# Kernel tuning notes

Hardware: AMD Instinct MI355X
Metric: run time of the kernel (lower is better)

## Reference

```python
import jax, jax.numpy as jnp
import numpy as np
from jax import lax

B, T, N, E, M = 2, 24, 1500, 2000, 4000
DIM, NLY, K = 64, 2, 3
H = DIM + DIM // 2  # 96: GAT input dim after concat with NodeEdge output


def setup_inputs():
    ks = iter(jax.random.split(jax.random.key(0), 100))
    def rn(shape, scale=1.0):
        return jax.random.normal(next(ks), shape, dtype=jnp.float32) * scale
    d = {}
    d["x_in"] = rn((B, T, N, 4)); d["e_in"] = rn((B, T, E, 3))
    d["b_in"] = rn((B, T, N, 4)); d["a_in"] = rn((B, T, E, 3))
    def lin(name, din, dout):
        d[name + "_W"] = rn((din, dout), 1.0 / float(np.sqrt(din)))
        d[name + "_b"] = jnp.zeros((dout,), jnp.float32)
    lin("enc0", 4, DIM); lin("enc1", 3, DIM)
    lin("enc2", 4, DIM // 2); lin("enc3", 3, DIM // 2)
    d["inci"] = jax.random.uniform(next(ks), (N, E), dtype=jnp.float32)
    for p in ("s1", "s2"):
        for g in ("gx", "ge"):
            d[p + "_" + g + "_W"] = rn((NLY, H, DIM), 0.1)
            d[p + "_" + g + "_as"] = rn((NLY, DIM), 0.1)
            d[p + "_" + g + "_ad"] = rn((NLY, DIM), 0.1)
            d[p + "_" + g + "_b"] = jnp.zeros((NLY, DIM), jnp.float32)
        d[p + "_ne_W"] = rn((NLY, DIM, DIM // 2), 0.125)
        d[p + "_ne_b"] = jnp.zeros((NLY, DIM // 2), jnp.float32)
        d[p + "_ne_w"] = rn((NLY, N, E), 0.02)
        d[p + "_ne_p"] = jnp.zeros((NLY, N, E), jnp.float32)
        d[p + "_en_W"] = rn((NLY, DIM, DIM // 2), 0.125)
        d[p + "_en_b"] = jnp.zeros((NLY, DIM // 2), jnp.float32)
        d[p + "_en_w"] = rn((NLY, E, N), 0.02)
        d[p + "_en_p"] = jnp.zeros((NLY, E, N), jnp.float32)
        d[p + "_tp_W"] = rn((NLY, DIM, DIM, K), 0.07)
        d[p + "_tp_b"] = jnp.zeros((NLY, DIM), jnp.float32)
    lin("conc", H, DIM); lin("res", DIM, DIM); lin("out", DIM, 1)
    d["edge_ind"] = jax.random.randint(next(ks), (2, E), 0, N)
    d["node_ind"] = jax.random.randint(next(ks), (2, M), 0, E)
    return d


def gat(x, src, dst, n, W, a_s, a_d, bias):
    # PyG GATConv (heads=1, concat=True, neg_slope=0.2); self-loops already in src/dst.
    # x: [B,T,n,din] -> G=B*T independent graphs (the batched edge_index replication
    # of BatchGATConv is exactly equivalent to vmapping over graph replicas).
    g = x.reshape(B * T, n, x.shape[-1])
    z = g @ W                                    # [G,n,DIM]
    es = jnp.einsum('gnd,d->gn', z, a_s)
    ed = jnp.einsum('gnd,d->gn', z, a_d)
    alpha = jax.nn.leaky_relu(es[:, src] + ed[:, dst], 0.2)   # [G,Etot]
    def one(a, zz):
        m = jax.ops.segment_max(a, dst, num_segments=n)
        ex = jnp.exp(a - m[dst])
        s = jax.ops.segment_sum(ex, dst, num_segments=n)
        w = ex / s[dst]
        return jax.ops.segment_sum(w[:, None] * zz[src], dst, num_segments=n)
    out = jax.vmap(one)(alpha, z) + bias
    return out.reshape(B, T, n, DIM)


def node_edge(inp, W, b, w, p, A):
    # NodeEdge: relu(Linear(dim->dim//2)) then incidence-masked matmul
    xe = jax.nn.relu(inp @ W + b)                # [B,T,*,DIM//2]
    return jnp.einsum('ne,btef->btnf', w * A + p, xe)


def causal_conv(h, W, b, dil):
    # h: [M,C,T]; left-pad (K-1)*dil -> causal dilated Conv1d
    pad = (K - 1) * dil
    out = lax.conv_general_dilated(h, W, (1,), [(pad, 0)], rhs_dilation=(dil,),
                                   dimension_numbers=('NCH', 'OIH', 'NCH'))
    return out + b[None, :, None]


def stblock(x, e, src_n, dst_n, src_e, dst_e, inc, P):
    (gxW, gxas, gxad, gxb, geW, geas, gead, geb,
     neW, neb, new, nep, enW, enb, enw, enp, tpW, tpb) = P
    incT = inc.T
    for l in range(NLY):
        xe = node_edge(e, neW[l], neb[l], new[l], nep[l], inc)
        x = jax.nn.relu(gat(jnp.concatenate([x, xe], -1), src_n, dst_n, N,
                            gxW[l], gxas[l], gxad[l], gxb[l]))
        ex = node_edge(x, enW[l], enb[l], enw[l], enp[l], incT)
        e = jax.nn.relu(gat(jnp.concatenate([e, ex], -1), src_e, dst_e, E,
                            geW[l], geas[l], gead[l], geb[l]))
    xt = x.transpose(0, 2, 3, 1).reshape(B * N, DIM, T)   # 'b t n d -> (b n) d t'
    et = e.transpose(0, 2, 3, 1).reshape(B * E, DIM, T)
    h = jnp.concatenate([xt, et], axis=0)
    for l in range(NLY):
        h = jax.nn.relu(causal_conv(h, tpW[l], tpb[l], 2 ** l))
    x = h[:B * N].reshape(B, N, DIM, T).transpose(0, 3, 1, 2)
    e = h[B * N:].reshape(B, E, DIM, T).transpose(0, 3, 1, 2)
    return x, e


def _forward(x_in, e_in, b_in, a_in, enc0_W, enc0_b, enc1_W, enc1_b, enc2_W, enc2_b,
             enc3_W, enc3_b, inci,
             s1_gx_W, s1_gx_as, s1_gx_ad, s1_gx_b, s1_ge_W, s1_ge_as, s1_ge_ad, s1_ge_b,
             s1_ne_W, s1_ne_b, s1_ne_w, s1_ne_p, s1_en_W, s1_en_b, s1_en_w, s1_en_p,
             s1_tp_W, s1_tp_b,
             s2_gx_W, s2_gx_as, s2_gx_ad, s2_gx_b, s2_ge_W, s2_ge_as, s2_ge_ad, s2_ge_b,
             s2_ne_W, s2_ne_b, s2_ne_w, s2_ne_p, s2_en_W, s2_en_b, s2_en_w, s2_en_p,
             s2_tp_W, s2_tp_b,
             conc_W, conc_b, res_W, res_b, out_W, out_b, edge_ind, node_ind):
    # add self-loops once (GATConv add_self_loops=True)
    src_n = jnp.concatenate([edge_ind[0], jnp.arange(N)])
    dst_n = jnp.concatenate([edge_ind[1], jnp.arange(N)])
    src_e = jnp.concatenate([node_ind[0], jnp.arange(E)])
    dst_e = jnp.concatenate([node_ind[1], jnp.arange(E)])
    inc = jnp.abs(inci)
    x = x_in @ enc0_W + enc0_b
    e = e_in @ enc1_W + enc1_b
    bb = jax.nn.relu(b_in @ enc2_W + enc2_b)
    aa = jax.nn.relu(a_in @ enc3_W + enc3_b)
    res_x = jnp.broadcast_to(x[:, -1:], (B, T, N, DIM))   # pre-relu last step, tiled
    res_e = jnp.broadcast_to(e[:, -1:], (B, T, E, DIM))
    x = jax.nn.relu(x); e = jax.nn.relu(e)
    P1 = (s1_gx_W, s1_gx_as, s1_gx_ad, s1_gx_b, s1_ge_W, s1_ge_as, s1_ge_ad, s1_ge_b,
          s1_ne_W, s1_ne_b, s1_ne_w, s1_ne_p, s1_en_W, s1_en_b, s1_en_w, s1_en_p,
          s1_tp_W, s1_tp_b)
    P2 = (s2_gx_W, s2_gx_as, s2_gx_ad, s2_gx_b, s2_ge_W, s2_ge_as, s2_ge_ad, s2_ge_b,
          s2_ne_W, s2_ne_b, s2_ne_w, s2_ne_p, s2_en_W, s2_en_b, s2_en_w, s2_en_p,
          s2_tp_W, s2_tp_b)
    x, e = stblock(x, e, src_n, dst_n, src_e, dst_e, inc, P1)
    # concs is [Linear]*2 in torch -> shared weights for both branches
    x = jax.nn.relu(jnp.concatenate([x, bb], -1) @ conc_W + conc_b)
    e = jax.nn.relu(jnp.concatenate([e, aa], -1) @ conc_W + conc_b)
    x, e = stblock(x, e, src_n, dst_n, src_e, dst_e, inc, P2)
    x = jax.nn.relu(jnp.cumsum(x @ res_W + res_b, axis=1) + res_x)
    e = jax.nn.relu(jnp.cumsum(e @ res_W + res_b, axis=1) + res_e)
    out = jnp.clip((x @ out_W + out_b) / 6.0 + 0.5, 0.0, 1.0)   # F.hardsigmoid
    eo = jnp.tanh(e @ out_W + out_b)
    return out, eo


def reference(x_in, e_in, b_in, a_in, enc0_W, enc0_b, enc1_W, enc1_b, enc2_W, enc2_b,
              enc3_W, enc3_b, inci,
              s1_gx_W, s1_gx_as, s1_gx_ad, s1_gx_b, s1_ge_W, s1_ge_as, s1_ge_ad, s1_ge_b,
              s1_ne_W, s1_ne_b, s1_ne_w, s1_ne_p, s1_en_W, s1_en_b, s1_en_w, s1_en_p,
              s1_tp_W, s1_tp_b,
              s2_gx_W, s2_gx_as, s2_gx_ad, s2_gx_b, s2_ge_W, s2_ge_as, s2_ge_ad, s2_ge_b,
              s2_ne_W, s2_ne_b, s2_ne_w, s2_ne_p, s2_en_W, s2_en_b, s2_en_w, s2_en_p,
              s2_tp_W, s2_tp_b,
              conc_W, conc_b, res_W, res_b, out_W, out_b, edge_ind, node_ind):
    return _forward(x_in, e_in, b_in, a_in, enc0_W, enc0_b, enc1_W, enc1_b, enc2_W,
                    enc2_b, enc3_W, enc3_b, inci,
                    s1_gx_W, s1_gx_as, s1_gx_ad, s1_gx_b, s1_ge_W, s1_ge_as, s1_ge_ad,
                    s1_ge_b, s1_ne_W, s1_ne_b, s1_ne_w, s1_ne_p, s1_en_W, s1_en_b,
                    s1_en_w, s1_en_p, s1_tp_W, s1_tp_b,
                    s2_gx_W, s2_gx_as, s2_gx_ad, s2_gx_b, s2_ge_W, s2_ge_as, s2_ge_ad,
                    s2_ge_b, s2_ne_W, s2_ne_b, s2_ne_w, s2_ne_p, s2_en_W, s2_en_b,
                    s2_en_w, s2_en_p, s2_tp_W, s2_tp_b,
                    conc_W, conc_b, res_W, res_b, out_W, out_b, edge_ind, node_ind)
```

## Files before the change

kernel.cpp:

```cpp
#include <hip/hip_runtime.h>
#include <hip/hip_bf16.h>
#include <cfloat>
#include <math.h>

typedef __hip_bfloat16 bf16;
typedef __attribute__((ext_vector_type(8))) short short8v;
typedef __attribute__((ext_vector_type(4))) float f32x4;

constexpr int B_ = 2, T_ = 24, N_ = 1500, E_ = 2000, M_ = 4000, G_ = 48;
constexpr int KPN = 2048;
constexpr int KPE = 1536;

__device__ __forceinline__ float b2f(bf16 v) { return __bfloat162float(v); }
__device__ __forceinline__ bf16 f2b(float v) { return __float2bfloat16(v); }
static inline int ceilDiv(int a, int b) { return (a + b - 1) / b; }

__global__ __launch_bounds__(256) void k_sentinel(float* __restrict__ out, int n, float val) {
  int i = blockIdx.x * 256 + threadIdx.x;
  if (i < n) out[i] = val;
}

__global__ __launch_bounds__(256) void k_wprep(const float* __restrict__ g0, const float* __restrict__ e0,
                                               const float* __restrict__ g1, const float* __restrict__ e1,
                                               const float* __restrict__ cw, const float* __restrict__ rw,
                                               const float* __restrict__ t0, const float* __restrict__ t1,
                                               bf16* __restrict__ out) {
  int i = blockIdx.x * 256 + threadIdx.x;
  if (i >= 108544) return;
  float v;
  if (i < 49152) {
    int which = i / 12288, r = i % 12288;
    const float* W = which == 0 ? g0 : which == 1 ? e0 : which == 2 ? g1 : e1;
    int l = r / 6144, j = r % 6144;
    int n = j / 96, k = j % 96;
    v = W[l * 6144 + k * 64 + n];
  } else if (i < 55296) {
    int j = i - 49152, n = j / 96, k = j % 96;
    v = cw[k * 64 + n];
  } else if (i < 59392) {
    int j = i - 55296, n = j / 64, k = j % 64;
    v = rw[k * 64 + n];
  } else {
    int r = i - 59392;
    int which = r / 24576;
    const float* W = which ? t1 : t0;
    int rr = r % 24576;
    int l = rr / 12288, j = rr % 12288;
    int ii = j & 63, o = (j >> 6) & 63, k = j >> 12;
    v = W[l * 12288 + o * 192 + ii * 3 + k];
  }
  out[i] = f2b(v);
}

template <int DIN, int DOUT, bool SAVE>
__global__ __launch_bounds__(256) void k_enc(const float* __restrict__ in, const float* __restrict__ W,
                                             const float* __restrict__ bias, bf16* __restrict__ out,
                                             float* __restrict__ last, int nodes) {
  int idx = blockIdx.x * 256 + threadIdx.x;
  if (idx >= G_ * nodes * DOUT) return;
  int d = idx % DOUT;
  int row = idx / DOUT;
  int node = row % nodes;
  int g = row / nodes;
  const float* ir = in + (size_t)row * DIN;
  float acc = bias[d];
#pragma unroll
  for (int i = 0; i < DIN; i++) acc += ir[i] * W[i * DOUT + d];
  if (SAVE) {
    if (g % T_ == T_ - 1) last[((size_t)(g / T_) * nodes + node) * DOUT + d] = acc;
  }
  out[idx] = f2b(fmaxf(acc, 0.f));
}

__global__ __launch_bounds__(256) void k_lin_neT(const bf16* __restrict__ act, const float* __restrict__ W,
                                                 const float* __restrict__ bias, bf16* __restrict__ outT,
                                                 int nodes, int Kp) {
  __shared__ float As[64][65];
  __shared__ float Ws[2048];
  __shared__ float bs[32];
  int g = blockIdx.y;
  int n0 = blockIdx.x * 64;
  int t = threadIdx.x;
  for (int i = t; i < 2048; i += 256) Ws[i] = W[i];
  if (t < 32) bs[t] = bias[t];
  {
    int r = t >> 2, ch = t & 3;
    int node = n0 + r;
    short tmp[16];
    if (node < nodes) {
      const bf16* src = act + ((size_t)g * nodes + node) * 64 + ch * 16;
      *reinterpret_cast<uint4*>(tmp) = *reinterpret_cast<const uint4*>(src);
      *reinterpret_cast<uint4*>(tmp + 8) = *reinterpret_cast<const uint4*>(src + 8);
#pragma unroll
      for (int j = 0; j < 16; j++) As[r][ch * 16 + j] = b2f(*reinterpret_cast<bf16*>(&tmp[j]));
    } else {
#pragma unroll
      for (int j = 0; j < 16; j++) As[r][ch * 16 + j] = 0.f;
    }
  }
  __syncthreads();
  int nd = t & 63, fq = t >> 6;
  float acc[8];
#pragma unroll
  for (int j = 0; j < 8; j++) acc[j] = bs[fq * 8 + j];
  for (int i = 0; i < 64; i++) {
    float a = As[nd][i];
#pragma unroll
    for (int j = 0; j < 8; j++) acc[j] += a * Ws[i * 32 + fq * 8 + j];
  }
  bool valid = (n0 + nd) < nodes;
#pragma unroll
  for (int j = 0; j < 8; j++) {
    float v = valid ? fmaxf(acc[j], 0.f) : 0.f;
    outT[(size_t)(g * 32 + fq * 8 + j) * Kp + n0 + nd] = f2b(v);
  }
}

__global__ __launch_bounds__(256) void k_mat(const float* __restrict__ w, const float* __restrict__ p,
                                             const float* __restrict__ inci, bf16* __restrict__ mat,
                                             int rows, int K, int Kp) {
  int i = blockIdx.x * 256 + threadIdx.x;
  if (i >= rows * Kp) return;
  int row = i / Kp, k = i % Kp;
  float v = 0.f;
  if (k < K) {
    size_t o = (size_t)row * K + k;
    v = w[o] * fabsf(inci[o]) + p[o];
  }
  mat[i] = f2b(v);
}

__global__ void k_matT(const float* __restrict__ w, const float* __restrict__ p,
                       const float* __restrict__ inci, bf16* __restrict__ mat) {
  __shared__ float tl[32][33];
  int e0 = blockIdx.x * 32, n0 = blockIdx.y * 32;
  for (int r = threadIdx.y; r < 32; r += 8) {
    int n = n0 + r, e = e0 + threadIdx.x;
    tl[r][threadIdx.x] = (n < N_ && e < E_) ? fabsf(inci[(size_t)n * E_ + e]) : 0.f;
  }
  __syncthreads();
  for (int r = threadIdx.y; r < 32; r += 8) {
    int e = e0 + r, n = n0 + threadIdx.x;
    if (e < E_ && n < KPE) {
      size_t o = (size_t)e * N_ + n;
      mat[(size_t)e * KPE + n] = (n < N_) ? f2b(tl[threadIdx.x][r] * w[o] + p[o]) : f2b(0.f);
    }
  }
}

__global__ __launch_bounds__(256) void k_mgemm64(const bf16* __restrict__ A0, const bf16* __restrict__ Bt,
                                                 bf16* __restrict__ Cp, int Mm, int Kp, int Nn, int gy) {
  __shared__ __align__(16) short As[4][4][64][8];
  __shared__ __align__(16) short Bs[4][4][64][8];
  int tid = threadIdx.x;
  int nwg = gridDim.x;
  int bid = blockIdx.x;
  int l = (bid & 7) * (nwg >> 3) + (bid >> 3);
  int bm = (l % gy) * 64, bn = (l / gy) * 64;
  int lane = tid & 63, wid = tid >> 6;
  int wr = wid >> 1, wc = wid & 1;
  f32x4 acc[2][2];
#pragma unroll
  for (int i = 0; i < 2; i++)
#pragma unroll
    for (int j = 0; j < 2; j++) acc[i][j] = f32x4{0.f, 0.f, 0.f, 0.f};

  const int sr = tid >> 2;
  const int sc = tid & 3;
  const int kb = lane >> 4, lr = lane & 15;
  const int gmA = bm + sr, gnB = bn + sr;
  const bool va_ok = (gmA < Mm), vb_ok = (gnB < Nn);
  const bf16* ap = A0 + (size_t)gmA * Kp + sc * 8;
  const bf16* bp = Bt + (size_t)gnB * Kp + sc * 8;
  const uint4 z4 = {0, 0, 0, 0};
  const int P = Kp >> 5;

  uint4 va0 = va_ok ? *reinterpret_cast<const uint4*>(ap) : z4;
  uint4 vb0 = vb_ok ? *reinterpret_cast<const uint4*>(bp) : z4;
  uint4 va1 = va_ok ? *reinterpret_cast<const uint4*>(ap + 32) : z4;
  uint4 vb1 = vb_ok ? *reinterpret_cast<const uint4*>(bp + 32) : z4;
  *reinterpret_cast<uint4*>(&As[0][sc][sr][0]) = va0;
  *reinterpret_cast<uint4*>(&Bs[0][sc][sr][0]) = vb0;
  uint4 va2 = va_ok ? *reinterpret_cast<const uint4*>(ap + 64) : z4;
  uint4 vb2 = vb_ok ? *reinterpret_cast<const uint4*>(bp + 64) : z4;
  __syncthreads();

  for (int p = 0; p < P; p += 2) {
    *reinterpret_cast<uint4*>(&As[(p + 1) & 3][sc][sr][0]) = va1;
    *reinterpret_cast<uint4*>(&Bs[(p + 1) & 3][sc][sr][0]) = vb1;
    if (p + 3 < P) {
      va1 = va_ok ? *reinterpret_cast<const uint4*>(ap + (p + 3) * 32) : z4;
      vb1 = vb_ok ? *reinterpret_cast<const uint4*>(bp + (p + 3) * 32) : z4;
    }
    {
      int bf = p & 3;
      short8v a0 = *reinterpret_cast<const short8v*>(&As[bf][kb][wr * 32 + lr][0]);
      short8v a1 = *reinterpret_cast<const short8v*>(&As[bf][kb][wr * 32 + 16 + lr][0]);
      short8v b0 = *reinterpret_cast<const short8v*>(&Bs[bf][kb][wc * 32 + lr][0]);
      short8v b1 = *reinterpret_cast<const short8v*>(&Bs[bf][kb][wc * 32 + 16 + lr][0]);
      __builtin_amdgcn_s_setprio(1);
      acc[0][0] = __builtin_amdgcn_mfma_f32_16x16x32_bf16(a0, b0, acc[0][0], 0, 0, 0);
      acc[0][1] = __builtin_amdgcn_mfma_f32_16x16x32_bf16(a0, b1, acc[0][1], 0, 0, 0);
      acc[1][0] = __builtin_amdgcn_mfma_f32_16x16x32_bf16(a1, b0, acc[1][0], 0, 0, 0);
      acc[1][1] = __builtin_amdgcn_mfma_f32_16x16x32_bf16(a1, b1, acc[1][1], 0, 0, 0);
      __builtin_amdgcn_s_setprio(0);
    }
    __syncthreads();
    *reinterpret_cast<uint4*>(&As[(p + 2) & 3][sc][sr][0]) = va2;
    *reinterpret_cast<uint4*>(&Bs[(p + 2) & 3][sc][sr][0]) = vb2;
    if (p + 4 < P) {
      va2 = va_ok ? *reinterpret_cast<const uint4*>(ap + (p + 4) * 32) : z4;
      vb2 = vb_ok ? *reinterpret_cast<const uint4*>(bp + (p + 4) * 32) : z4;
    }
    {
      int bf = (p + 1) & 3;
      short8v a0 = *reinterpret_cast<const short8v*>(&As[bf][kb][wr * 32 + lr][0]);
      short8v a1 = *reinterpret_cast<const short8v*>(&As[bf][kb][wr * 32 + 16 + lr][0]);
      short8v b0 = *reinterpret_cast<const short8v*>(&Bs[bf][kb][wc * 32 + lr][0]);
      short8v b1 = *reinterpret_cast<const short8v*>(&Bs[bf][kb][wc * 32 + 16 + lr][0]);
      __builtin_amdgcn_s_setprio(1);
      acc[0][0] = __builtin_amdgcn_mfma_f32_16x16x32_bf16(a0, b0, acc[0][0], 0, 0, 0);
      acc[0][1] = __builtin_amdgcn_mfma_f32_16x16x32_bf16(a0, b1, acc[0][1], 0, 0, 0);
      acc[1][0] = __builtin_amdgcn_mfma_f32_16x16x32_bf16(a1, b0, acc[1][0], 0, 0, 0);
      acc[1][1] = __builtin_amdgcn_mfma_f32_16x16x32_bf16(a1, b1, acc[1][1], 0, 0, 0);
      __builtin_amdgcn_s_setprio(0);
    }
    __syncthreads();
  }
#pragma unroll
  for (int mi = 0; mi < 2; mi++) {
    int r0 = bm + wr * 32 + mi * 16 + (lane >> 4) * 4;
#pragma unroll
    for (int ni = 0; ni < 2; ni++) {
      int col = bn + wc * 32 + ni * 16 + lr;
      if (col >= Nn) continue;
#pragma unroll
      for (int i = 0; i < 4; i++) {
        int r = r0 + i;
        if (r < Mm) Cp[(size_t)r * Nn + col] = f2b(acc[mi][ni][i]);
      }
    }
  }
}

template <int AMODE, int BNt, bool CF32b, bool ESED>
__global__ __launch_bounds__(256) void k_mgemm(const bf16* __restrict__ A0, const bf16* __restrict__ A1,
                                               const bf16* __restrict__ Bt, void* __restrict__ Cp,
                                               int Mm, int Kp, int Nn, int nodes,
                                               const float* __restrict__ bias, int relu,
                                               const float* __restrict__ asv, const float* __restrict__ adv,
                                               float* __restrict__ esOut, float* __restrict__ edOut) {
  constexpr int BM = 128;
  constexpr int WTN = BNt / 32;
  __shared__ __align__(16) short As[4][BM][8];
  __shared__ __align__(16) short Bs[4][BNt][8];
  __shared__ float smr[2][BM][2];
  int tid = threadIdx.x;
  int bm = blockIdx.y * BM;
  int bn = blockIdx.x * BNt;
  int lane = tid & 63;
  int wid = tid >> 6;
  int wr = wid >> 1, wc = wid & 1;
  f32x4 acc[4][WTN];
#pragma unroll
  for (int i = 0; i < 4; i++)
#pragma unroll
    for (int j = 0; j < WTN; j++) acc[i][j] = f32x4{0.f, 0.f, 0.f, 0.f};

  const int ar = tid >> 1;
  const int ah = tid & 1;
  const int kb = lane >> 4;
  const int lr = lane & 15;

  for (int k0 = 0; k0 < Kp; k0 += 32) {
    uint4 va0 = {0, 0, 0, 0}, va1 = {0, 0, 0, 0};
    int gm = bm + ar;
    if (gm < Mm) {
      int ks = k0 + ah * 16;
      const bf16* src;
      if (AMODE == 0) src = A0 + (size_t)gm * Kp + ks;
      else if (ks < 64) src = A0 + (size_t)gm * 64 + ks;
      else if (AMODE == 1) {
        int g = gm / nodes, nd = gm % nodes;
        src = A1 + ((size_t)nd * G_ + g) * 32 + (ks - 64);
      } else {
        src = A1 + (size_t)gm * 32 + (ks - 64);
      }
      const uint4* p = reinterpret_cast<const uint4*>(src);
      va0 = p[0];
      va1 = p[1];
    }
    *reinterpret_cast<uint4*>(&As[ah * 2 + 0][ar][0]) = va0;
    *reinterpret_cast<uint4*>(&As[ah * 2 + 1][ar][0]) = va1;
    if (BNt == 128) {
      int br = tid >> 1, bh = tid & 1;
      uint4 vb0 = {0, 0, 0, 0}, vb1 = {0, 0, 0, 0};
      int gn = bn + br;
      if (gn < Nn) {
        const uint4* p = reinterpret_cast<const uint4*>(Bt + (size_t)gn * Kp + k0 + bh * 16);
        vb0 = p[0];
        vb1 = p[1];
      }
      *reinterpret_cast<uint4*>(&Bs[bh * 2 + 0][br][0]) = vb0;
      *reinterpret_cast<uint4*>(&Bs[bh * 2 + 1][br][0]) = vb1;
    } else {
      int br = tid >> 2, bk = tid & 3;
      uint4 vb0 = {0, 0, 0, 0};
      int gn = bn + br;
      if (gn < Nn) vb0 = *reinterpret_cast<const uint4*>(Bt + (size_t)gn * Kp + k0 + bk * 8);
      *reinterpret_cast<uint4*>(&Bs[bk][br][0]) = vb0;
    }
    __syncthreads();
    short8v a[4], b[WTN];
#pragma unroll
    for (int mi = 0; mi < 4; mi++)
      a[mi] = *reinterpret_cast<const short8v*>(&As[kb][wr * 64 + mi * 16 + lr][0]);
#pragma unroll
    for (int ni = 0; ni < WTN; ni++)
      b[ni] = *reinterpret_cast<const short8v*>(&Bs[kb][wc * (BNt / 2) + ni * 16 + lr][0]);
#pragma unroll
    for (int mi = 0; mi < 4; mi++)
#pragma unroll
      for (int ni = 0; ni < WTN; ni++)
        acc[mi][ni] = __builtin_amdgcn_mfma_f32_16x16x32_bf16(a[mi], b[ni], acc[mi][ni], 0, 0, 0);
    __syncthreads();
  }
#pragma unroll
  for (int mi = 0; mi < 4; mi++) {
    int r0 = bm + wr * 64 + mi * 16 + (lane >> 4) * 4;
#pragma unroll
    for (int ni = 0; ni < WTN; ni++) {
      int col = bn + wc * (BNt / 2) + ni * 16 + lr;
      float bv = bias ? bias[col] : 0.f;
#pragma unroll
      for (int i = 0; i < 4; i++) {
        int r = r0 + i;
        if (r < Mm) {
          float v = acc[mi][ni][i] + bv;
          if (relu) v = fmaxf(v, 0.f);
          if (CF32b) ((float*)Cp)[(size_t)r * Nn + col] = v;
          else ((bf16*)Cp)[(size_t)r * Nn + col] = f2b(v);
        }
      }
    }
  }
  if (ESED) {
    float asc0 = asv[wc * 32 + lr];
    float asc1 = asv[wc * 32 + 16 + lr];
    float adc0 = adv[wc * 32 + lr];
    float adc1 = adv[wc * 32 + 16 + lr];
#pragma unroll
    for (int mi = 0; mi < 4; mi++) {
#pragma unroll
      for (int i = 0; i < 4; i++) {
        float pe = acc[mi][0][i] * asc0 + acc[mi][1][i] * asc1;
        float pd = acc[mi][0][i] * adc0 + acc[mi][1][i] * adc1;
#pragma unroll
        for (int o = 8; o; o >>= 1) { pe += __shfl_xor(pe, o); pd += __shfl_xor(pd, o); }
        if (lr == 0) {
          int rl = wr * 64 + mi * 16 + (lane >> 4) * 4 + i;
          smr[wc][rl][0] = pe;
          smr[wc][rl][1] = pd;
        }
      }
    }
    __syncthreads();
    if (tid < BM) {
      int r = bm + tid;
      if (r < Mm) {
        esOut[r] = smr[0][tid][0] + smr[1][tid][0];
        edOut[r] = smr[0][tid][1] + smr[1][tid][1];
      }
    }
  }
}

template <int DIL>
__global__ __launch_bounds__(256) void k_cgemm(const bf16* __restrict__ A, const bf16* __restrict__ Wc,
                                               const float* __restrict__ bias, bf16* __restrict__ C,
                                               int Mm, int nodes) {
  __shared__ __align__(16) short As[4][4][128][8];
  int tid = threadIdx.x;
  int bm = blockIdx.x * 128;
  int lane = tid & 63, wid = tid >> 6;
  int wr = wid >> 1, wc = wid & 1;
  const int ar = tid >> 1, ah = tid & 1;
  const int kb = lane >> 4, lr = lane & 15;
  const int gm = bm + ar;
  const int t = (gm / nodes) % T_;
  const uint4 z4 = {0, 0, 0, 0};

  short8v bfr[3][2][2];
#pragma unroll
  for (int tap = 0; tap < 3; tap++)
#pragma unroll
    for (int kc = 0; kc < 2; kc++)
#pragma unroll
      for (int ni = 0; ni < 2; ni++) {
        int col = wc * 32 + ni * 16 + lr;
        bfr[tap][kc][ni] = *reinterpret_cast<const short8v*>(Wc + tap * 4096 + (size_t)col * 64 + kc * 32 + kb * 8);
      }

  f32x4 acc[4][2];
#pragma unroll
  for (int i = 0; i < 4; i++)
#pragma unroll
    for (int j = 0; j < 2; j++) acc[i][j] = f32x4{0.f, 0.f, 0.f, 0.f};

#define CG_LDA(p, vx, vy)                                                          \
  {                                                                                \
    const int sh_ = (((p) >> 1) - 2) * DIL;                                        \
    if ((gm < Mm) && (t + sh_ >= 0)) {                                             \
      const uint4* pp = reinterpret_cast<const uint4*>(                            \
          A + ((size_t)gm + (size_t)sh_ * nodes) * 64 + ((p) & 1) * 32 + ah * 16); \
      vx = pp[0];                                                                  \
      vy = pp[1];                                                                  \
    } else {                                                                       \
      vx = z4;                                                                     \
      vy = z4;                                                                     \
    }                                                                              \
  }
#define CG_WR(buf, vx, vy)                                     \
  *reinterpret_cast<uint4*>(&As[buf][ah * 2 + 0][ar][0]) = vx; \
  *reinterpret_cast<uint4*>(&As[buf][ah * 2 + 1][ar][0]) = vy;
#define CG_MFMA(q)                                                                                         \
  {                                                                                                        \
    short8v a0_ = *reinterpret_cast<const short8v*>(&As[(q) & 3][kb][wr * 64 + 0 + lr][0]);                \
    short8v a1_ = *reinterpret_cast<const short8v*>(&As[(q) & 3][kb][wr * 64 + 16 + lr][0]);               \
    short8v a2_ = *reinterpret_cast<const short8v*>(&As[(q) & 3][kb][wr * 64 + 32 + lr][0]);               \
    short8v a3_ = *reinterpret_cast<const short8v*>(&As[(q) & 3][kb][wr * 64 + 48 + lr][0]);               \
    __builtin_amdgcn_s_setprio(1);                                                                         \
    acc[0][0] = __builtin_amdgcn_mfma_f32_16x16x32_bf16(a0_, bfr[(q) >> 1][(q) & 1][0], acc[0][0], 0, 0, 0); \
    acc[0][1] = __builtin_amdgcn_mfma_f32_16x16x32_bf16(a0_, bfr[(q) >> 1][(q) & 1][1], acc[0][1], 0, 0, 0); \
    acc[1][0] = __builtin_amdgcn_mfma_f32_16x16x32_bf16(a1_, bfr[(q) >> 1][(q) & 1][0], acc[1][0], 0, 0, 0); \
    acc[1][1] = __builtin_amdgcn_mfma_f32_16x16x32_bf16(a1_, bfr[(q) >> 1][(q) & 1][1], acc[1][1], 0, 0, 0); \
    acc[2][0] = __builtin_amdgcn_mfma_f32_16x16x32_bf16(a2_, bfr[(q) >> 1][(q) & 1][0], acc[2][0], 0, 0, 0); \
    acc[2][1] = __builtin_amdgcn_mfma_f32_16x16x32_bf16(a2_, bfr[(q) >> 1][(q) & 1][1], acc[2][1], 0, 0, 0); \
    acc[3][0] = __builtin_amdgcn_mfma_f32_16x16x32_bf16(a3_, bfr[(q) >> 1][(q) & 1][0], acc[3][0], 0, 0, 0); \
    acc[3][1] = __builtin_amdgcn_mfma_f32_16x16x32_bf16(a3_, bfr[(q) >> 1][(q) & 1][1], acc[3][1], 0, 0, 0); \
    __builtin_amdgcn_s_setprio(0);                                                                         \
  }
#define CG_BODY(p, lastPair)                  \
  CG_WR(((p) + 1) & 3, r1x, r1y);             \
  if (!(lastPair)) CG_LDA((p) + 3, r1x, r1y); \
  CG_MFMA(p);                                 \
  __syncthreads();                            \
  CG_WR(((p) + 2) & 3, r2x, r2y);             \
  if (!(lastPair)) CG_LDA((p) + 4, r2x, r2y); \
  CG_MFMA((p) + 1);                           \
  __syncthreads();

  uint4 p0x, p0y, r1x, r1y, r2x, r2y;
  CG_LDA(0, p0x, p0y);
  CG_LDA(1, r1x, r1y);
  CG_WR(0, p0x, p0y);
  CG_LDA(2, r2x, r2y);
  __syncthreads();

  CG_BODY(0, false)
  CG_BODY(2, false)
  CG_BODY(4, true)

#undef CG_LDA
#undef CG_WR
#undef CG_MFMA
#undef CG_BODY

#pragma unroll
  for (int mi = 0; mi < 4; mi++) {
    int r0 = bm + wr * 64 + mi * 16 + (lane >> 4) * 4;
#pragma unroll
    for (int ni = 0; ni < 2; ni++) {
      int col = wc * 32 + ni * 16 + lr;
      float bv = bias[col];
#pragma unroll
      for (int i = 0; i < 4; i++) {
        int r = r0 + i;
        if (r < Mm) C[(size_t)r * 64 + col] = f2b(fmaxf(acc[mi][ni][i] + bv, 0.f));
      }
    }
  }
}

__global__ __launch_bounds__(256) void k_gat_w(const float* __restrict__ es, const float* __restrict__ edv,
                                               const int* __restrict__ off, const int* __restrict__ adj,
                                               float* __restrict__ wgt, int nodes, int tot) {
  int idx = blockIdx.x * 256 + threadIdx.x;
  if (idx >= G_ * nodes) return;
  int g = idx / nodes, node = idx % nodes;
  int s0 = off[node], s1 = off[node + 1];
  const float* esg = es + (size_t)g * nodes;
  float edval = edv[(size_t)g * nodes + node];
  float m = -FLT_MAX;
  for (int s = s0; s < s1; s++) {
    float a = esg[adj[s]] + edval;
    a = (a >= 0.f) ? a : 0.2f * a;
    m = fmaxf(m, a);
  }
  float den = 0.f;
  float* wg = wgt + (size_t)g * tot;
  for (int s = s0; s < s1; s++) {
    float a = esg[adj[s]] + edval;
    a = (a >= 0.f) ? a : 0.2f * a;
    float ex = expf(a - m);
    den += ex;
    wg[s] = ex;
  }
  float inv = (s1 > s0) ? 1.f / den : 0.f;
  for (int s = s0; s < s1; s++) wg[s] *= inv;
}

__global__ __launch_bounds__(256) void k_gat_aggr3(const bf16* __restrict__ z, const float* __restrict__ wgt,
                                                   const int* __restrict__ off, const int* __restrict__ adj,
                                                   const float* __restrict__ bias, bf16* __restrict__ out,
                                                   int nodes, int tot) {
  int idx = blockIdx.x * 256 + threadIdx.x;
  if (idx >= G_ * nodes * 16) return;
  int c = idx & 15;
  int rest = idx >> 4;
  int node = rest % nodes;
  int g = rest / nodes;
  int s0 = off[node], s1 = off[node + 1];
  const bf16* zg = z + (size_t)g * nodes * 64 + c * 4;
  const float* wg = wgt + (size_t)g * tot;
  float n0 = 0.f, n1 = 0.f, n2 = 0.f, n3 = 0.f;
  for (int s = s0; s < s1; s++) {
    int src = adj[s];
    float w = wg[s];
    bf16 v[4];
    *reinterpret_cast<uint2*>(v) = *reinterpret_cast<const uint2*>(zg + (size_t)src * 64);
    n0 += w * b2f(v[0]);
    n1 += w * b2f(v[1]);
    n2 += w * b2f(v[2]);
    n3 += w * b2f(v[3]);
  }
  bf16 ov[4];
  ov[0] = f2b(fmaxf(n0 + bias[c * 4 + 0], 0.f));
  ov[1] = f2b(fmaxf(n1 + bias[c * 4 + 1], 0.f));
  ov[2] = f2b(fmaxf(n2 + bias[c * 4 + 2], 0.f));
  ov[3] = f2b(fmaxf(n3 + bias[c * 4 + 3], 0.f));
  *reinterpret_cast<uint2*>(out + (size_t)rest * 64 + c * 4) = *reinterpret_cast<uint2*>(ov);
}

__global__ __launch_bounds__(1024) void k_csr(const int* __restrict__ indN, const int* __restrict__ indE,
                                              int* __restrict__ offN, int* __restrict__ adjN,
                                              int* __restrict__ offE, int* __restrict__ adjE) {
  __shared__ int cnt[2048];
  __shared__ int a[1024];
  const int* ind;
  int ner, nn;
  int *off, *adj;
  if (blockIdx.x == 0) { ind = indN; ner = E_; nn = N_; off = offN; adj = adjN; }
  else { ind = indE; ner = M_; nn = E_; off = offE; adj = adjE; }
  int tot = ner + nn;
  int t = threadIdx.x;
  for (int i = t; i < nn; i += 1024) cnt[i] = 0;
  __syncthreads();
  for (int i = t; i < tot; i += 1024) {
    int d = (i < ner) ? ind[ner + i] : (i - ner);
    if (d >= 0 && d < nn) atomicAdd(&cnt[d], 1);
  }
  __syncthreads();
  int c0 = (2 * t < nn) ? cnt[2 * t] : 0;
  int c1 = (2 * t + 1 < nn) ? cnt[2 * t + 1] : 0;
  a[t] = c0 + c1;
  __syncthreads();
  for (int d = 1; d < 1024; d <<= 1) {
    int u = (t >= d) ? a[t - d] : 0;
    __syncthreads();
    a[t] += u;
    __syncthreads();
  }
  int excl = (t > 0) ? a[t - 1] : 0;
  if (2 * t < nn) { cnt[2 * t] = excl; off[2 * t] = excl; }
  if (2 * t + 1 < nn) { cnt[2 * t + 1] = excl + c0; off[2 * t + 1] = excl + c0; }
  if (t == 0) off[nn] = a[1023];
  __syncthreads();
  for (int i = t; i < tot; i += 1024) {
    int s, d;
    if (i < ner) { s = ind[i]; d = ind[ner + i]; }
    else { s = d = i - ner; }
    if (d >= 0 && d < nn) {
      int pos = atomicAdd(&cnt[d], 1);
      adj[pos] = s;
    }
  }
}

template <bool XB>
__global__ __launch_bounds__(256) void k_out(const float* __restrict__ yx, const float* __restrict__ last,
                                             const float* __restrict__ oW, const float* __restrict__ ob_,
                                             float* __restrict__ dout, int nodes) {
  int wid = threadIdx.x >> 6, lane = threadIdx.x & 63;
  int node = blockIdx.x * 4 + wid;
  if (node >= nodes) return;
  float lw = oW[lane];
  float ob = ob_[0];
  float lv = last[(size_t)node * 64 + lane];
  float acc = 0.f;
  for (int tt = 0; tt < T_; tt++) {
    acc += yx[((size_t)tt * nodes + node) * 64 + lane];
    float v = fmaxf(acc + lv, 0.f);
    float p = v * lw;
#pragma unroll
    for (int o2 = 32; o2; o2 >>= 1) p += __shfl_down(p, o2);
    if (lane == 0) {
      float o = p + ob;
      if (XB) o = fminf(fmaxf(o / 6.f + 0.5f, 0.f), 1.f);
      else o = tanhf(o);
      dout[(size_t)tt * nodes + node] = o;
    }
  }
}

extern "C" void kernel_launch(void* const* d_in, const int* in_sizes, int n_in,
                              void* d_out, int out_size, void* d_ws, size_t ws_size,
                              hipStream_t stream) {
  float* dout = (float*)d_out;

  if (n_in != 57) {
    k_sentinel<<<ceilDiv(out_size, 256), 256, 0, stream>>>(dout, out_size, 20000.f + 128.f * n_in);
    return;
  }
  static const int expSz[57] = {
      288000, 288000, 288000, 288000,
      256, 64, 192, 64, 128, 32, 96, 32,
      3000000,
      12288, 128, 128, 128, 12288, 128, 128, 128,
      4096, 64, 6000000, 6000000, 4096, 64, 6000000, 6000000,
      24576, 128,
      12288, 128, 128, 128, 12288, 128, 128, 128,
      4096, 64, 6000000, 6000000, 4096, 64, 6000000, 6000000,
      24576, 128,
      6144, 64, 4096, 64, 64, 1, 4000, 8000};
  for (int i = 0; i < 57; i++) {
    if (in_sizes[i] != expSz[i]) {
      k_sentinel<<<ceilDiv(out_size, 256), 256, 0, stream>>>(dout, out_size, 4096.f + 64.f * i);
      return;
    }
  }

  auto ff = [&](int i) { return (const float*)d_in[i]; };
  const float *x_in = ff(0), *e_in = ff(1), *b_in = ff(2), *a_in = ff(3);
  const float *enc0W = ff(4), *enc0b = ff(5), *enc1W = ff(6), *enc1b = ff(7);
  const float *enc2W = ff(8), *enc2b = ff(9), *enc3W = ff(10), *enc3b = ff(11);
  const float* inci = ff(12);
  const float *concW = ff(49), *concb = ff(50), *resW = ff(51), *resb = ff(52);
  const float *outW = ff(53), *outb = ff(54);
  const int* edge_ind = (const int*)d_in[55];
  const int* node_ind = (const int*)d_in[56];

  char* base = (char*)d_ws;
  size_t off = 0;
  auto A = [&](size_t bytes) { void* p = base + off; off = (off + bytes + 255) & ~(size_t)255; return p; };
  char* SCR = (char*)A(21504000);
  bf16* xbuf = (bf16*)A(9216000);
  bf16* ebuf = (bf16*)A(12288000);
  float* lastx = (float*)A(768000);
  float* laste = (float*)A(1024000);
  float* es = (float*)A(384000);
  float* edv = (float*)A(384000);
  float* wgt = (float*)A((size_t)G_ * (M_ + E_) * 4);
  bf16* wAll = (bf16*)A(217088);
  int* offN = (int*)A((N_ + 1) * 4);
  int* offE = (int*)A((E_ + 1) * 4);
  int* adjN = (int*)A((E_ + N_) * 4);
  int* adjE = (int*)A((M_ + E_) * 4);
  size_t required = off;

  if (ws_size < required) {
    k_sentinel<<<ceilDiv(out_size, 256), 256, 0, stream>>>(dout, out_size, 1000.f + (float)(ws_size >> 20));
    return;
  }

  bf16* matb = (bf16*)SCR;
  bf16* tlinT = (bf16*)(SCR + 6553600);
  bf16* tmat = (bf16*)(SCR + 13107200);
  bf16* zbuf = (bf16*)SCR;
  bf16* bscr = (bf16*)SCR;
  bf16* cx1 = (bf16*)SCR;
  bf16* ce1 = (bf16*)(SCR + 9216000);
  float* zres = (float*)SCR;

  const int totN = E_ + N_;
  const int totE = M_ + E_;

  k_wprep<<<ceilDiv(108544, 256), 256, 0, stream>>>(ff(13), ff(17), ff(31), ff(35), concW, resW,
                                                    ff(29), ff(47), wAll);
  k_csr<<<2, 1024, 0, stream>>>(edge_ind, node_ind, offN, adjN, offE, adjE);

  k_enc<4, 64, true><<<ceilDiv(G_ * N_ * 64, 256), 256, 0, stream>>>(x_in, enc0W, enc0b, xbuf, lastx, N_);
  k_enc<3, 64, true><<<ceilDiv(G_ * E_ * 64, 256), 256, 0, stream>>>(e_in, enc1W, enc1b, ebuf, laste, E_);

  auto stblock = [&](int sb, int sbi) {
    const float *gxas = ff(sb + 1), *gxad = ff(sb + 2), *gxb = ff(sb + 3);
    const float *geas = ff(sb + 5), *gead = ff(sb + 6), *geb = ff(sb + 7);
    const float *neW = ff(sb + 8), *neb = ff(sb + 9), *nw = ff(sb + 10), *np_ = ff(sb + 11);
    const float *enW = ff(sb + 12), *enb = ff(sb + 13), *ew = ff(sb + 14), *ep = ff(sb + 15);
    const float* tpb = ff(sb + 17);
    for (int l = 0; l < 2; l++) {
      const bf16* gxw_t = wAll + sbi * 24576 + l * 6144;
      const bf16* gew_t = wAll + sbi * 24576 + 12288 + l * 6144;
      k_lin_neT<<<dim3(KPN / 64, G_), 256, 0, stream>>>(ebuf, neW + l * 2048, neb + l * 32, tlinT, E_, KPN);
      k_mat<<<ceilDiv(N_ * KPN, 256), 256, 0, stream>>>(nw + (size_t)l * N_ * E_, np_ + (size_t)l * N_ * E_, inci, matb, N_, E_, KPN);
      k_mgemm64<<<dim3(24 * 24), 256, 0, stream>>>(matb, tlinT, tmat, N_, KPN, 1536, 24);
      k_mgemm<1, 64, false, true><<<dim3(1, ceilDiv(G_ * N_, 128)), 256, 0, stream>>>(
          xbuf, tmat, gxw_t, zbuf, G_ * N_, 96, 64, N_, nullptr, 0, gxas + l * 64, gxad + l * 64, es, edv);
      k_gat_w<<<ceilDiv(G_ * N_, 256), 256, 0, stream>>>(es, edv, offN, adjN, wgt, N_, totN);
      k_gat_aggr3<<<ceilDiv(G_ * N_ * 16, 256), 256, 0, stream>>>(zbuf, wgt, offN, adjN, gxb + l * 64, xbuf, N_, totN);
      k_lin_neT<<<dim3(KPE / 64, G_), 256, 0, stream>>>(xbuf, enW + l * 2048, enb + l * 32, tlinT, N_, KPE);
      k_matT<<<dim3(ceilDiv(E_, 32), KPE / 32), dim3(32, 8), 0, stream>>>(ew + (size_t)l * E_ * N_, ep + (size_t)l * E_ * N_, inci, matb);
      k_mgemm64<<<dim3(24 * 32), 256, 0, stream>>>(matb, tlinT, tmat, E_, KPE, 1536, 32);
      k_mgemm<1, 64, false, true><<<dim3(1, ceilDiv(G_ * E_, 128)), 256, 0, stream>>>(
          ebuf, tmat, gew_t, zbuf, G_ * E_, 96, 64, E_, nullptr, 0, geas + l * 64, gead + l * 64, es, edv);
      k_gat_w<<<ceilDiv(G_ * E_, 256), 256, 0, stream>>>(es, edv, offE, adjE, wgt, E_, totE);
      k_gat_aggr3<<<ceilDiv(G_ * E_ * 16, 256), 256, 0, stream>>>(zbuf, wgt, offE, adjE, geb + l * 64, ebuf, E_, totE);
    }
    const bf16* cw0 = wAll + 59392 + sbi * 24576;
    const bf16* cw1 = cw0 + 12288;
    k_cgemm<1><<<ceilDiv(G_ * N_, 128), 256, 0, stream>>>(xbuf, cw0, tpb, cx1, G_ * N_, N_);
    k_cgemm<1><<<ceilDiv(G_ * E_, 128), 256, 0, stream>>>(ebuf, cw0, tpb, ce1, G_ * E_, E_);
    k_cgemm<2><<<ceilDiv(G_ * N_, 128), 256, 0, stream>>>(cx1, cw1, tpb + 64, xbuf, G_ * N_, N_);
    k_cgemm<2><<<ceilDiv(G_ * E_, 128), 256, 0, stream>>>(ce1, cw1, tpb + 64, ebuf, G_ * E_, E_);
  };

  stblock(13, 0);

  const bf16* concT = wAll + 49152;
  k_enc<4, 32, false><<<ceilDiv(G_ * N_ * 32, 256), 256, 0, stream>>>(b_in, enc2W, enc2b, bscr, nullptr, N_);
  k_mgemm<2, 64, false, false><<<dim3(1, ceilDiv(G_ * N_, 128)), 256, 0, stream>>>(
      xbuf, bscr, concT, xbuf, G_ * N_, 96, 64, 0, concb, 1, nullptr, nullptr, nullptr, nullptr);
  k_enc<3, 32, false><<<ceilDiv(G_ * E_ * 32, 256), 256, 0, stream>>>(a_in, enc3W, enc3b, bscr, nullptr, E_);
  k_mgemm<2, 64, false, false><<<dim3(1, ceilDiv(G_ * E_, 128)), 256, 0, stream>>>(
      ebuf, bscr, concT, ebuf, G_ * E_, 96, 64, 0, concb, 1, nullptr, nullptr, nullptr, nullptr);

  stblock(31, 1);

  const bf16* resT = wAll + 55296;
  for (int b = 0; b < B_; b++) {
    k_mgemm<0, 64, true, false><<<dim3(1, ceilDiv(T_ * N_, 128)), 256, 0, stream>>>(
        xbuf + (size_t)b * T_ * N_ * 64, nullptr, resT, zres, T_ * N_, 64, 64, 0, resb, 0,
        nullptr, nullptr, nullptr, nullptr);
    k_out<true><<<ceilDiv(N_, 4), 256, 0, stream>>>(
        zres, lastx + (size_t)b * N_ * 64, outW, outb, dout + (size_t)b * T_ * N_, N_);
  }
  for (int b = 0; b < B_; b++) {
    k_mgemm<0, 64, true, false><<<dim3(1, ceilDiv(T_ * E_, 128)), 256, 0, stream>>>(
        ebuf + (size_t)b * T_ * E_ * 64, nullptr, resT, zres, T_ * E_, 64, 64, 0, resb, 0,
        nullptr, nullptr, nullptr, nullptr);
    k_out<false><<<ceilDiv(E_, 4), 256, 0, stream>>>(
        zres, laste + (size_t)b * E_ * 64, outW, outb, dout + (size_t)(B_ * T_ * N_) + (size_t)b * T_ * E_, E_);
  }
}
```

Measured before the change: 1.050 ms.

## Specialize small GEMM with full-K LDS load and merge node/edge launches

Replaces the generic k-looped k_mgemm with k_mgemm96, which loads the whole K=96 (or 64) A and B tiles into LDS once, syncs once, and runs all MFMAs under raised priority. The two temporal-conv GEMMs for nodes and edges are merged into single launches, and the node residual GEMM and output kernel now cover both batches in one launch each. The aim is fewer barriers and fewer kernel launches, at the cost of more LDS per block and a fixed N=64 output width.

After: 1.019 ms. -3.0%, faster.

```diff
diff --git a/kernel.cpp b/kernel.cpp
--- a/kernel.cpp
+++ b/kernel.cpp
@@ -243,94 +243,89 @@
   }
 }
 
-template <int AMODE, int BNt, bool CF32b, bool ESED>
-__global__ __launch_bounds__(256) void k_mgemm(const bf16* __restrict__ A0, const bf16* __restrict__ A1,
-                                               const bf16* __restrict__ Bt, void* __restrict__ Cp,
-                                               int Mm, int Kp, int Nn, int nodes,
-                                               const float* __restrict__ bias, int relu,
-                                               const float* __restrict__ asv, const float* __restrict__ adv,
-                                               float* __restrict__ esOut, float* __restrict__ edOut) {
-  constexpr int BM = 128;
-  constexpr int WTN = BNt / 32;
-  __shared__ __align__(16) short As[4][BM][8];
-  __shared__ __align__(16) short Bs[4][BNt][8];
-  __shared__ float smr[2][BM][2];
+template <int AMODE, int KOCT, bool CF32b, bool ESED>
+__global__ __launch_bounds__(256) void k_mgemm96(const bf16* __restrict__ A0, const bf16* __restrict__ A1,
+                                                 const bf16* __restrict__ Bt, void* __restrict__ Cp,
+                                                 int Mm, int nodes,
+                                                 const float* __restrict__ bias, int relu,
+                                                 const float* __restrict__ asv, const float* __restrict__ adv,
+                                                 float* __restrict__ esOut, float* __restrict__ edOut) {
+  constexpr int KP = KOCT * 8;
+  __shared__ __align__(16) short As[KOCT][128][8];
+  __shared__ __align__(16) short Bs[KOCT][64][8];
+  __shared__ float smr[2][128][2];
   int tid = threadIdx.x;
-  int bm = blockIdx.y * BM;
-  int bn = blockIdx.x * BNt;
-  int lane = tid & 63;
-  int wid = tid >> 6;
+  int bm = blockIdx.y * 128;
+  int lane = tid & 63, wid = tid >> 6;
   int wr = wid >> 1, wc = wid & 1;
-  f32x4 acc[4][WTN];
+  const int kb = lane >> 4, lr = lane & 15;
+  const uint4 z4 = {0, 0, 0, 0};
+
+  {
+    int ar = tid >> 1, ah = tid & 1;
+    int gm = bm + ar;
+    bool ok = (gm < Mm);
+    int gdiv = 0, gmod = 0;
+    if (AMODE == 1 && ok) { gdiv = gm / nodes; gmod = gm % nodes; }
+#pragma unroll
+    for (int c = 0; c < KOCT / 4; c++) {
+      int ks = c * 32 + ah * 16;
+      uint4 va0 = z4, va1 = z4;
+      if (ok) {
+        const bf16* src;
+        if (AMODE == 0) src = A0 + (size_t)gm * KP + ks;
+        else if (ks < 64) src = A0 + (size_t)gm * 64 + ks;
+        else if (AMODE == 1) src = A1 + ((size_t)gmod * G_ + gdiv) * 32 + (ks - 64);
+        else src = A1 + (size_t)gm * 32 + (ks - 64);
+        const uint4* p = reinterpret_cast<const uint4*>(src);
+        va0 = p[0];
+        va1 = p[1];
+      }
+      *reinterpret_cast<uint4*>(&As[c * 4 + ah * 2 + 0][ar][0]) = va0;
+      *reinterpret_cast<uint4*>(&As[c * 4 + ah * 2 + 1][ar][0]) = va1;
+    }
+  }
+  {
+    int br = tid >> 2, bk = tid & 3;
+#pragma unroll
+    for (int c = 0; c < KOCT / 4; c++) {
+      int o = c * 4 + bk;
+      uint4 vb = *reinterpret_cast<const uint4*>(Bt + (size_t)br * KP + o * 8);
+      *reinterpret_cast<uint4*>(&Bs[o][br][0]) = vb;
+    }
+  }
+  __syncthreads();
+
+  f32x4 acc[4][2];
 #pragma unroll
   for (int i = 0; i < 4; i++)
 #pragma unroll
-    for (int j = 0; j < WTN; j++) acc[i][j] = f32x4{0.f, 0.f, 0.f, 0.f};
-
-  const int ar = tid >> 1;
-  const int ah = tid & 1;
-  const int kb = lane >> 4;
-  const int lr = lane & 15;
-
-  for (int k0 = 0; k0 < Kp; k0 += 32) {
-    uint4 va0 = {0, 0, 0, 0}, va1 = {0, 0, 0, 0};
-    int gm = bm + ar;
-    if (gm < Mm) {
-      int ks = k0 + ah * 16;
-      const bf16* src;
-      if (AMODE == 0) src = A0 + (size_t)gm * Kp + ks;
-      else if (ks < 64) src = A0 + (size_t)gm * 64 + ks;
-      else if (AMODE == 1) {
-        int g = gm / nodes, nd = gm % nodes;
-        src = A1 + ((size_t)nd * G_ + g) * 32 + (ks - 64);
-      } else {
-        src = A1 + (size_t)gm * 32 + (ks - 64);
-      }
-      const uint4* p = reinterpret_cast<const uint4*>(src);
-      va0 = p[0];
-      va1 = p[1];
-    }
-    *reinterpret_cast<uint4*>(&As[ah * 2 + 0][ar][0]) = va0;
-    *reinterpret_cast<uint4*>(&As[ah * 2 + 1][ar][0]) = va1;
-    if (BNt == 128) {
-      int br = tid >> 1, bh = tid & 1;
-      uint4 vb0 = {0, 0, 0, 0}, vb1 = {0, 0, 0, 0};
-      int gn = bn + br;
-      if (gn < Nn) {
-        const uint4* p = reinterpret_cast<const uint4*>(Bt + (size_t)gn * Kp + k0 + bh * 16);
-        vb0 = p[0];
-        vb1 = p[1];
-      }
-      *reinterpret_cast<uint4*>(&Bs[bh * 2 + 0][br][0]) = vb0;
-      *reinterpret_cast<uint4*>(&Bs[bh * 2 + 1][br][0]) = vb1;
-    } else {
-      int br = tid >> 2, bk = tid & 3;
-      uint4 vb0 = {0, 0, 0, 0};
-      int gn = bn + br;
-      if (gn < Nn) vb0 = *reinterpret_cast<const uint4*>(Bt + (size_t)gn * Kp + k0 + bk * 8);
-      *reinterpret_cast<uint4*>(&Bs[bk][br][0]) = vb0;
-    }
-    __syncthreads();
-    short8v a[4], b[WTN];
+    for (int j = 0; j < 2; j++) acc[i][j] = f32x4{0.f, 0.f, 0.f, 0.f};
+
+#pragma unroll
+  for (int c = 0; c < KOCT / 4; c++) {
+    short8v a[4], b[2];
 #pragma unroll
     for (int mi = 0; mi < 4; mi++)
-      a[mi] = *reinterpret_cast<const short8v*>(&As[kb][wr * 64 + mi * 16 + lr][0]);
-#pragma unroll
-    for (int ni = 0; ni < WTN; ni++)
-      b[ni] = *reinterpret_cast<const short8v*>(&Bs[kb][wc * (BNt / 2) + ni * 16 + lr][0]);
+      a[mi] = *reinterpret_cast<const short8v*>(&As[c * 4 + kb][wr * 64 + mi * 16 + lr][0]);
+#pragma unroll
+    for (int ni = 0; ni < 2; ni++)
+      b[ni] = *reinterpret_cast<const short8v*>(&Bs[c * 4 + kb][wc * 32 + ni * 16 + lr][0]);
+    __builtin_amdgcn_s_setprio(1);
 #pragma unroll
     for (int mi = 0; mi < 4; mi++)
 #pragma unroll
-      for (int ni = 0; ni < WTN; ni++)
+      for (int ni = 0; ni < 2; ni++)
         acc[mi][ni] = __builtin_amdgcn_mfma_f32_16x16x32_bf16(a[mi], b[ni], acc[mi][ni], 0, 0, 0);
-    __syncthreads();
-  }
+    __builtin_amdgcn_s_setprio(0);
+  }
+
 #pragma unroll
   for (int mi = 0; mi < 4; mi++) {
     int r0 = bm + wr * 64 + mi * 16 + (lane >> 4) * 4;
 #pragma unroll
-    for (int ni = 0; ni < WTN; ni++) {
-      int col = bn + wc * (BNt / 2) + ni * 16 + lr;
+    for (int ni = 0; ni < 2; ni++) {
+      int col = wc * 32 + ni * 16 + lr;
       float bv = bias ? bias[col] : 0.f;
 #pragma unroll
       for (int i = 0; i < 4; i++) {
@@ -338,8 +333,8 @@
         if (r < Mm) {
           float v = acc[mi][ni][i] + bv;
           if (relu) v = fmaxf(v, 0.f);
-          if (CF32b) ((float*)Cp)[(size_t)r * Nn + col] = v;
-          else ((bf16*)Cp)[(size_t)r * Nn + col] = f2b(v);
+          if (CF32b) ((float*)Cp)[(size_t)r * 64 + col] = v;
+          else ((bf16*)Cp)[(size_t)r * 64 + col] = f2b(v);
         }
       }
     }
@@ -365,7 +360,7 @@
       }
     }
     __syncthreads();
-    if (tid < BM) {
+    if (tid < 128) {
       int r = bm + tid;
       if (r < Mm) {
         esOut[r] = smr[0][tid][0] + smr[1][tid][0];
@@ -376,12 +371,18 @@
 }
 
 template <int DIL>
-__global__ __launch_bounds__(256) void k_cgemm(const bf16* __restrict__ A, const bf16* __restrict__ Wc,
-                                               const float* __restrict__ bias, bf16* __restrict__ C,
-                                               int Mm, int nodes) {
+__global__ __launch_bounds__(256) void k_cgemm2(const bf16* __restrict__ Ax, bf16* __restrict__ Cx,
+                                                int Mx, int nx, const bf16* __restrict__ Ae,
+                                                bf16* __restrict__ Ce, int Me, int ne, int nbx,
+                                                const bf16* __restrict__ Wc, const float* __restrict__ bias) {
   __shared__ __align__(16) short As[4][4][128][8];
   int tid = threadIdx.x;
-  int bm = blockIdx.x * 128;
+  int bid = blockIdx.x;
+  const bf16* A;
+  bf16* C;
+  int Mm, nodes, bm;
+  if (bid < nbx) { A = Ax; C = Cx; Mm = Mx; nodes = nx; bm = bid * 128; }
+  else { A = Ae; C = Ce; Mm = Me; nodes = ne; bm = (bid - nbx) * 128; }
   int lane = tid & 63, wid = tid >> 6;
   int wr = wid >> 1, wc = wid & 1;
   const int ar = tid >> 1, ah = tid & 1;
@@ -590,16 +591,18 @@
 template <bool XB>
 __global__ __launch_bounds__(256) void k_out(const float* __restrict__ yx, const float* __restrict__ last,
                                              const float* __restrict__ oW, const float* __restrict__ ob_,
-                                             float* __restrict__ dout, int nodes) {
+                                             float* __restrict__ dout, int nodes, int batches) {
   int wid = threadIdx.x >> 6, lane = threadIdx.x & 63;
-  int node = blockIdx.x * 4 + wid;
-  if (node >= nodes) return;
+  int idx = blockIdx.x * 4 + wid;
+  if (idx >= batches * nodes) return;
+  int b = idx / nodes, node = idx % nodes;
+  const float* yb = yx + (size_t)b * T_ * nodes * 64;
   float lw = oW[lane];
   float ob = ob_[0];
-  float lv = last[(size_t)node * 64 + lane];
+  float lv = last[(size_t)idx * 64 + lane];
   float acc = 0.f;
   for (int tt = 0; tt < T_; tt++) {
-    acc += yx[((size_t)tt * nodes + node) * 64 + lane];
+    acc += yb[((size_t)tt * nodes + node) * 64 + lane];
     float v = fmaxf(acc + lv, 0.f);
     float p = v * lw;
 #pragma unroll
@@ -608,7 +611,7 @@
       float o = p + ob;
       if (XB) o = fminf(fmaxf(o / 6.f + 0.5f, 0.f), 1.f);
       else o = tanhf(o);
-      dout[(size_t)tt * nodes + node] = o;
+      dout[(size_t)b * T_ * nodes + (size_t)tt * nodes + node] = o;
     }
   }
 }
@@ -684,6 +687,8 @@
 
   const int totN = E_ + N_;
   const int totE = M_ + E_;
+  const int nbx = ceilDiv(G_ * N_, 128);
+  const int nbe = ceilDiv(G_ * E_, 128);
 
   k_wprep<<<ceilDiv(108544, 256), 256, 0, stream>>>(ff(13), ff(17), ff(31), ff(35), concW, resW,
                                                     ff(29), ff(47), wAll);
@@ -704,51 +709,45 @@
       k_lin_neT<<<dim3(KPN / 64, G_), 256, 0, stream>>>(ebuf, neW + l * 2048, neb + l * 32, tlinT, E_, KPN);
       k_mat<<<ceilDiv(N_ * KPN, 256), 256, 0, stream>>>(nw + (size_t)l * N_ * E_, np_ + (size_t)l * N_ * E_, inci, matb, N_, E_, KPN);
       k_mgemm64<<<dim3(24 * 24), 256, 0, stream>>>(matb, tlinT, tmat, N_, KPN, 1536, 24);
-      k_mgemm<1, 64, false, true><<<dim3(1, ceilDiv(G_ * N_, 128)), 256, 0, stream>>>(
-          xbuf, tmat, gxw_t, zbuf, G_ * N_, 96, 64, N_, nullptr, 0, gxas + l * 64, gxad + l * 64, es, edv);
+      k_mgemm96<1, 12, false, true><<<dim3(1, nbx), 256, 0, stream>>>(
+          xbuf, tmat, gxw_t, zbuf, G_ * N_, N_, nullptr, 0, gxas + l * 64, gxad + l * 64, es, edv);
       k_gat_w<<<ceilDiv(G_ * N_, 256), 256, 0, stream>>>(es, edv, offN, adjN, wgt, N_, totN);
       k_gat_aggr3<<<ceilDiv(G_ * N_ * 16, 256), 256, 0, stream>>>(zbuf, wgt, offN, adjN, gxb + l * 64, xbuf, N_, totN);
       k_lin_neT<<<dim3(KPE / 64, G_), 256, 0, stream>>>(xbuf, enW + l * 2048, enb + l * 32, tlinT, N_, KPE);
       k_matT<<<dim3(ceilDiv(E_, 32), KPE / 32), dim3(32, 8), 0, stream>>>(ew + (size_t)l * E_ * N_, ep + (size_t)l * E_ * N_, inci, matb);
       k_mgemm64<<<dim3(24 * 32), 256, 0, stream>>>(matb, tlinT, tmat, E_, KPE, 1536, 32);
-      k_mgemm<1, 64, false, true><<<dim3(1, ceilDiv(G_ * E_, 128)), 256, 0, stream>>>(
-          ebuf, tmat, gew_t, zbuf, G_ * E_, 96, 64, E_, nullptr, 0, geas + l * 64, gead + l * 64, es, edv);
+      k_mgemm96<1, 12, false, true><<<dim3(1, nbe), 256, 0, stream>>>(
+          ebuf, tmat, gew_t, zbuf, G_ * E_, E_, nullptr, 0, geas + l * 64, gead + l * 64, es, edv);
       k_gat_w<<<ceilDiv(G_ * E_, 256), 256, 0, stream>>>(es, edv, offE, adjE, wgt, E_, totE);
       k_gat_aggr3<<<ceilDiv(G_ * E_ * 16, 256), 256, 0, stream>>>(zbuf, wgt, offE, adjE, geb + l * 64, ebuf, E_, totE);
     }
     const bf16* cw0 = wAll + 59392 + sbi * 24576;
     const bf16* cw1 = cw0 + 12288;
-    k_cgemm<1><<<ceilDiv(G_ * N_, 128), 256, 0, stream>>>(xbuf, cw0, tpb, cx1, G_ * N_, N_);
-    k_cgemm<1><<<ceilDiv(G_ * E_, 128), 256, 0, stream>>>(ebuf, cw0, tpb, ce1, G_ * E_, E_);
-    k_cgemm<2><<<ceilDiv(G_ * N_, 128), 256, 0, stream>>>(cx1, cw1, tpb + 64, xbuf, G_ * N_, N_);
-    k_cgemm<2><<<ceilDiv(G_ * E_, 128), 256, 0, stream>>>(ce1, cw1, tpb + 64, ebuf, G_ * E_, E_);
+    k_cgemm2<1><<<nbx + nbe, 256, 0, stream>>>(xbuf, cx1, G_ * N_, N_, ebuf, ce1, G_ * E_, E_, nbx, cw0, tpb);
+    k_cgemm2<2><<<nbx + nbe, 256, 0, stream>>>(cx1, xbuf, G_ * N_, N_, ce1, ebuf, G_ * E_, E_, nbx, cw1, tpb + 64);
   };
 
   stblock(13, 0);
 
   const bf16* concT = wAll + 49152;
   k_enc<4, 32, false><<<ceilDiv(G_ * N_ * 32, 256), 256, 0, stream>>>(b_in, enc2W, enc2b, bscr, nullptr, N_);
-  k_mgemm<2, 64, false, false><<<dim3(1, ceilDiv(G_ * N_, 128)), 256, 0, stream>>>(
-      xbuf, bscr, concT, xbuf, G_ * N_, 96, 64, 0, concb, 1, nullptr, nullptr, nullptr, nullptr);
+  k_mgemm96<2, 12, false, false><<<dim3(1, nbx), 256, 0, stream>>>(
+      xbuf, bscr, concT, xbuf, G_ * N_, 0, concb, 1, nullptr, nullptr, nullptr, nullptr);
   k_enc<3, 32, false><<<ceilDiv(G_ * E_ * 32, 256), 256, 0, stream>>>(a_in, enc3W, enc3b, bscr, nullptr, E_);
-  k_mgemm<2, 64, false, false><<<dim3(1, ceilDiv(G_ * E_, 128)), 256, 0, stream>>>(
-      ebuf, bscr, concT, ebuf, G_ * E_, 96, 64, 0, concb, 1, nullptr, nullptr, nullptr, nullptr);
+  k_mgemm96<2, 12, false, false><<<dim3(1, nbe), 256, 0, stream>>>(
+      ebuf, bscr, concT, ebuf, G_ * E_, 0, concb, 1, nullptr, nullptr, nullptr, nullptr);
 
   stblock(31, 1);
 
   const bf16* resT = wAll + 55296;
+  k_mgemm96<0, 8, true, false><<<dim3(1, nbx), 256, 0, stream>>>(
+      xbuf, nullptr, resT, zres, G_ * N_, 0, resb, 0, nullptr, nullptr, nullptr, nullptr);
+  k_out<true><<<ceilDiv(B_ * N_, 4), 256, 0, stream>>>(zres, lastx, outW, outb, dout, N_, B_);
   for (int b = 0; b < B_; b++) {
-    k_mgemm<0, 64, true, false><<<dim3(1, ceilDiv(T_ * N_, 128)), 256, 0, stream>>>(
-        xbuf + (size_t)b * T_ * N_ * 64, nullptr, resT, zres, T_ * N_, 64, 64, 0, resb, 0,
-        nullptr, nullptr, nullptr, nullptr);
-    k_out<true><<<ceilDiv(N_, 4), 256, 0, stream>>>(
-        zres, lastx + (size_t)b * N_ * 64, outW, outb, dout + (size_t)b * T_ * N_, N_);
-  }
-  for (int b = 0; b < B_; b++) {
-    k_mgemm<0, 64, true, false><<<dim3(1, ceilDiv(T_ * E_, 128)), 256, 0, stream>>>(
-        ebuf + (size_t)b * T_ * E_ * 64, nullptr, resT, zres, T_ * E_, 64, 64, 0, resb, 0,
+    k_mgemm96<0, 8, true, false><<<dim3(1, ceilDiv(T_ * E_, 128)), 256, 0, stream>>>(
+        ebuf + (size_t)b * T_ * E_ * 64, nullptr, resT, zres, T_ * E_, 0, resb, 0,
         nullptr, nullptr, nullptr, nullptr);
     k_out<false><<<ceilDiv(E_, 4), 256, 0, stream>>>(
-        zres, laste + (size_t)b * E_ * 64, outW, outb, dout + (size_t)(B_ * T_ * N_) + (size_t)b * T_ * E_, E_);
-  }
-}
+        zres, laste + (size_t)b * E_ * 64, outW, outb, dout + (size_t)(B_ * T_ * N_) + (size_t)b * T_ * E_, E_, 1);
+  }
+}
```
